# Performance work log

Measured on AMD Instinct MI355X. Metric: run time of the kernel, lower is better.

Reference implementation:

```python
import jax, jax.numpy as jnp
import numpy as np

EPS = 1e-6
LOG2PI = float(np.log(2.0 * np.pi))


def gauss_lp(x, mu, lv):
    """Diagonal Gaussian log prob. x:[B,D], mu:[K,D], lv:[K,D] -> [B,K]."""
    inv_var = jnp.exp(-lv)                          # [K,D]
    d = x[:, None, :] - mu[None, :, :]              # [B,K,D]
    quad = jnp.sum(d * d * inv_var[None], axis=-1)  # [B,K]
    logdet = jnp.sum(lv, axis=-1)[None]             # [1,K]
    D = mu.shape[-1]
    return -0.5 * (quad + logdet + D * LOG2PI)


def setup_inputs() -> dict:
    key = jax.random.key(0)
    ks = jax.random.split(key, 9)
    T, B, S, A, OBS, CTL = 200, 256, 256, 16, 128, 16
    return {
        "x": jax.random.normal(ks[0], (T, B, OBS), jnp.float32),
        "u": jax.random.normal(ks[1], (T, B, CTL), jnp.float32),
        "obs_mu": jax.random.normal(ks[2], (S, OBS), jnp.float32),
        "obs_lv": 0.1 * jax.random.normal(ks[3], (S, OBS), jnp.float32),
        "ctl_mu": jax.random.normal(ks[4], (A, CTL), jnp.float32),
        "ctl_lv": 0.1 * jax.random.normal(ks[5], (A, CTL), jnp.float32),
        "trans_logits": jax.random.normal(ks[6], (A, S, S), jnp.float32),
        "pi0_logits": jax.random.normal(ks[7], (S,), jnp.float32),
        "act_prior": jax.random.normal(ks[8], (S, A), jnp.float32),
    }


def reference(x, u, obs_mu, obs_lv, ctl_mu, ctl_lv, trans_logits, pi0_logits, act_prior):
    """HMM forward algorithm (ContinuousGaussianHMM._forward).

    Returns:
      alpha_b: [T, B, S] state forward messages
      alpha_a: [T-1, B, A] action forward messages
    """
    S = obs_mu.shape[0]
    trans = jax.nn.softmax(trans_logits, axis=-1)      # [A,S,S]
    log_pi0 = jax.nn.log_softmax(pi0_logits)           # [S]

    # t = 0: initial state prior + observation likelihood
    b0 = jax.nn.softmax(gauss_lp(x[0], obs_mu, obs_lv) + log_pi0[None], axis=-1)  # [B,S]

    def step(b, xu):
        x_t, u_t = xu
        # action prior from belief: softmax(b @ act_prior)
        a_prior = jax.nn.softmax(b @ act_prior, axis=-1)                           # [B,A]
        # ctl_model.infer: posterior over actions given control u_t
        a_t = jax.nn.softmax(gauss_lp(u_t, ctl_mu, ctl_lv) + jnp.log(a_prior + EPS), axis=-1)  # [B,A]
        # action-conditioned transition applied to belief
        m = jnp.einsum('bi,kij->bkj', b, trans)                                    # [B,A,S]
        # original: sum_i(trans*b + eps) => einsum + S*eps
        logp_z = jnp.log(jnp.einsum('bk,bkj->bj', a_t, m) + S * EPS)               # [B,S]
        b_next = jax.nn.softmax(gauss_lp(x_t, obs_mu, obs_lv) + logp_z, axis=-1)   # [B,S]
        return b_next, (b_next, a_t)

    _, (bs, a_s) = jax.lax.scan(step, b0, (x[1:], u[:-1]))
    alpha_b = jnp.concatenate([b0[None], bs], axis=0)   # [T,B,S]
    alpha_a = a_s                                       # [T-1,B,A]
    return alpha_b, alpha_a
```

## Files before the change

### kernel.cpp

```cpp
#include <hip/hip_runtime.h>
#include <hip/hip_bf16.h>
#include <stdint.h>

#define T_STEPS 200
#define BATCH   256
#define NS      256
#define NA      16
#define DOBS    128
#define DCTL    16
#define LOG2PI  1.8378770664093453f
#define EPS_F   1e-6f

typedef float f32x4 __attribute__((ext_vector_type(4)));
typedef short s16x8 __attribute__((ext_vector_type(8)));
typedef short s16x4 __attribute__((ext_vector_type(4)));

static __device__ __forceinline__ unsigned short f2bf(float f) {
    union { float f; unsigned u; } v; v.f = f;
    unsigned u = v.u;
    u += 0x7fffu + ((u >> 16) & 1u);
    return (unsigned short)(u >> 16);
}

static __device__ __forceinline__ float ld_agent(const float* p) {
    return __hip_atomic_load(p, __ATOMIC_RELAXED, __HIP_MEMORY_SCOPE_AGENT);
}
static __device__ __forceinline__ void st_agent(float* p, float v) {
    __hip_atomic_store(p, v, __ATOMIC_RELAXED, __HIP_MEMORY_SCOPE_AGENT);
}

__global__ __launch_bounds__(128) void k_prep_obs(const float* __restrict__ obs_mu,
                                                  const float* __restrict__ obs_lv,
                                                  float* __restrict__ WT,
                                                  float* __restrict__ Cs) {
    int s = blockIdx.x, d = threadIdx.x;
    float lv = obs_lv[s * DOBS + d];
    float mu = obs_mu[s * DOBS + d];
    float iv = expf(-lv);
    WT[d * NS + s]          = -0.5f * iv;
    WT[(DOBS + d) * NS + s] = mu * iv;
    float part = mu * mu * iv + lv;
    for (int m = 1; m < 64; m <<= 1) part += __shfl_xor(part, m, 64);
    __shared__ float red[2];
    if ((threadIdx.x & 63) == 0) red[threadIdx.x >> 6] = part;
    __syncthreads();
    if (threadIdx.x == 0) Cs[s] = -0.5f * (red[0] + red[1] + DOBS * LOG2PI);
}

__global__ __launch_bounds__(256) void k_prep_ctl(const float* __restrict__ cmu,
                                                  const float* __restrict__ clv,
                                                  float* __restrict__ cw1,
                                                  float* __restrict__ cw2,
                                                  float* __restrict__ cc) {
    int t = threadIdx.x;
    int a = t >> 4, d = t & 15;
    float lv = clv[a * DCTL + d];
    float mu = cmu[a * DCTL + d];
    float iv = expf(-lv);
    cw1[t] = -0.5f * iv;
    cw2[t] = mu * iv;
    float part = mu * mu * iv + lv;
    for (int m = 1; m < 16; m <<= 1) part += __shfl_xor(part, m, 64);
    if (d == 0) cc[a] = -0.5f * (part + DCTL * LOG2PI);
}

__global__ __launch_bounds__(64) void k_prep_pi0(const float* __restrict__ pl,
                                                 float* __restrict__ lpi0) {
    int l = threadIdx.x;
    float v[4]; float m = -1e30f;
    for (int k = 0; k < 4; k++) { v[k] = pl[l + 64 * k]; m = fmaxf(m, v[k]); }
    for (int mm = 1; mm < 64; mm <<= 1) m = fmaxf(m, __shfl_xor(m, mm, 64));
    float ssum = 0.f;
    for (int k = 0; k < 4; k++) ssum += expf(v[k] - m);
    for (int mm = 1; mm < 64; mm <<= 1) ssum += __shfl_xor(ssum, mm, 64);
    float ls = logf(ssum);
    for (int k = 0; k < 4; k++) lpi0[l + 64 * k] = v[k] - m - ls;
}

__global__ __launch_bounds__(512) void k_zero(int* __restrict__ f) {
    f[threadIdx.x] = 0;
}

__global__ __launch_bounds__(256) void k_trans(const float* __restrict__ tl,
                                               __hip_bfloat16* __restrict__ TRf) {
    int wave = threadIdx.x >> 6, lane = threadIdx.x & 63;
    int row = blockIdx.x * 4 + wave;
    int a = row >> 8, i = row & 255;
    const float* src = tl + (size_t)row * NS;
    float v[4]; float m = -1e30f;
    for (int k = 0; k < 4; k++) { v[k] = src[lane + 64 * k]; m = fmaxf(m, v[k]); }
    for (int mm = 1; mm < 64; mm <<= 1) m = fmaxf(m, __shfl_xor(m, mm, 64));
    float ssum = 0.f; float ev[4];
    for (int k = 0; k < 4; k++) { ev[k] = expf(v[k] - m); ssum += ev[k]; }
    for (int mm = 1; mm < 64; mm <<= 1) ssum += __shfl_xor(ssum, mm, 64);
    float inv = 1.f / ssum;
    int kk = i >> 5;
    int lsub = ((i >> 3) & 3) * 16 + a;
    int e = i & 7;
    for (int k = 0; k < 4; k++) {
        int j = lane + 64 * k;
        float p = ev[k] * inv;
        TRf[((size_t)(j * 8 + kk) * 64 + lsub) * 8 + e] = __float2bfloat16(p);
    }
}

__global__ __launch_bounds__(64) void k_prep_ap(const float* __restrict__ ap,
                                                __hip_bfloat16* __restrict__ APh,
                                                __hip_bfloat16* __restrict__ APl) {
    int kk = blockIdx.x, lane = threadIdx.x;
    for (int e = 0; e < 8; e++) {
        int i = kk * 32 + (lane >> 4) * 8 + e;
        int a = lane & 15;
        float v = ap[i * NA + a];
        __hip_bfloat16 hb = __float2bfloat16(v);
        float hi = __bfloat162float(hb);
        APh[(kk * 64 + lane) * 8 + e] = hb;
        APl[(kk * 64 + lane) * 8 + e] = __float2bfloat16(v - hi);
    }
}

__global__ __launch_bounds__(256) void k_obslp(const float* __restrict__ x,
                                               const float* __restrict__ WT,
                                               const float* __restrict__ Cs,
                                               float* __restrict__ obs) {
    __shared__ float f[32 * 256];
    int r0 = blockIdx.x * 32;
    for (int idx = threadIdx.x; idx < 32 * DOBS; idx += 256) {
        int r = idx >> 7, d = idx & 127;
        float v = x[(size_t)(r0 + r) * DOBS + d];
        f[r * 256 + d] = v * v;
        f[r * 256 + 128 + d] = v;
    }
    __syncthreads();
    int s = threadIdx.x;
    float acc[32];
#pragma unroll
    for (int r = 0; r < 32; r++) acc[r] = 0.f;
    for (int d4 = 0; d4 < 64; d4++) {
        float w0 = WT[(d4 * 4 + 0) * NS + s];
        float w1 = WT[(d4 * 4 + 1) * NS + s];
        float w2 = WT[(d4 * 4 + 2) * NS + s];
        float w3 = WT[(d4 * 4 + 3) * NS + s];
#pragma unroll
        for (int r = 0; r < 32; r++) {
            f32x4 fv = *reinterpret_cast<const f32x4*>(&f[r * 256 + d4 * 4]);
            acc[r] += fv.x * w0 + fv.y * w1 + fv.z * w2 + fv.w * w3;
        }
    }
    float c = Cs[s];
#pragma unroll
    for (int r = 0; r < 32; r++) obs[(size_t)(r0 + r) * NS + s] = acc[r] + c;
}

__global__ __launch_bounds__(256) void k_ctllp(const float* __restrict__ u,
                                               const float* __restrict__ cw1,
                                               const float* __restrict__ cw2,
                                               const float* __restrict__ cc,
                                               float* __restrict__ ctl) {
    int idx = blockIdx.x * 256 + threadIdx.x;
    int r = idx >> 4, a = idx & 15;
    const float* ur = u + (size_t)r * DCTL;
    const float* w1 = cw1 + a * DCTL;
    const float* w2 = cw2 + a * DCTL;
    float acc = cc[a];
#pragma unroll
    for (int d = 0; d < 16; d++) {
        float uv = ur[d];
        acc += uv * uv * w1[d] + uv * w2[d];
    }
    ctl[idx] = acc;
}

struct ScanArgs {
    const float* obs;
    const float* ctlp;
    const float* lpi0;
    const __hip_bfloat16* TRf;
    const __hip_bfloat16* APh;
    const __hip_bfloat16* APl;
    float* lgA;
    float* lgB;
    float* out_ab;
    float* out_aa;
    int*   flags;
};

__global__ __launch_bounds__(256, 1) void k_scan_p(ScanArgs A) {
    const int bid  = blockIdx.x;
    const int bt   = bid >> 4;
    const int jt   = bid & 15;
    const int tid  = threadIdx.x;
    const int wv   = tid >> 6, lane = tid & 63;
    const int kgrp = lane >> 4, arow = lane & 15;
    const int b0   = bt * 16;
    int* flag = A.flags + bt * 32;

    __shared__ short AFL[8][16][32];

    s16x8 bfr[4][8];
#pragma unroll
    for (int q = 0; q < 4; q++) {
        int ct = jt * 16 + wv * 4 + q;
#pragma unroll
        for (int kk = 0; kk < 8; kk++)
            bfr[q][kk] = *((const s16x8*)A.TRf + (size_t)(ct * 8 + kk) * 64 + lane);
    }
    s16x8 aph[8], apl[8];
#pragma unroll
    for (int kk = 0; kk < 8; kk++) {
        aph[kk] = *((const s16x8*)A.APh + kk * 64 + lane);
        apl[kk] = *((const s16x8*)A.APl + kk * 64 + lane);
    }
    f32x4 lp0 = *(const f32x4*)&A.lpi0[lane * 4];

    for (int s = 0; s < T_STEPS - 1; s++) {
        const float* lin = (s & 1) ? A.lgB : A.lgA;
        float*       lout = (s & 1) ? A.lgA : A.lgB;

        float obs_pf[16];
#pragma unroll
        for (int q2 = 0; q2 < 4; q2++)
#pragma unroll
            for (int r = 0; r < 4; r++)
                obs_pf[q2 * 4 + r] =
                    A.obs[((size_t)(s + 1) * BATCH + b0 + kgrp * 4 + r) * NS + jt * 16 + wv * 4 + q2];

        if (s > 0) {
            if (tid == 0) {
                int tgt = 16 * s;
                while (__hip_atomic_load(flag, __ATOMIC_RELAXED, __HIP_MEMORY_SCOPE_AGENT) < tgt)
                    __builtin_amdgcn_s_sleep(2);
            }
            __syncthreads();
        }

        float vr[4][4];
        if (s == 0) {
#pragma unroll
            for (int q = 0; q < 4; q++) {
                int bb = b0 + wv * 4 + q;
                f32x4 o = *(const f32x4*)&A.obs[(size_t)bb * NS + lane * 4];
                vr[q][0] = o.x + lp0.x; vr[q][1] = o.y + lp0.y;
                vr[q][2] = o.z + lp0.z; vr[q][3] = o.w + lp0.w;
            }
        } else {
#pragma unroll
            for (int q = 0; q < 4; q++) {
                const float* rp = &lin[(size_t)(b0 + wv * 4 + q) * NS + lane * 4];
#pragma unroll
                for (int k = 0; k < 4; k++) vr[q][k] = ld_agent(rp + k);
            }
        }
#pragma unroll
        for (int q = 0; q < 4; q++) {
            int r = wv * 4 + q, bb = b0 + r;
            float m = fmaxf(fmaxf(vr[q][0], vr[q][1]), fmaxf(vr[q][2], vr[q][3]));
            for (int mm = 1; mm < 64; mm <<= 1) m = fmaxf(m, __shfl_xor(m, mm, 64));
            float e0 = __expf(vr[q][0] - m), e1 = __expf(vr[q][1] - m);
            float e2 = __expf(vr[q][2] - m), e3 = __expf(vr[q][3] - m);
            float ss = (e0 + e1) + (e2 + e3);
            for (int mm = 1; mm < 64; mm <<= 1) ss += __shfl_xor(ss, mm, 64);
            float inv = 1.f / ss;
            float p0 = e0 * inv, p1 = e1 * inv, p2 = e2 * inv, p3 = e3 * inv;
            if ((lane >> 2) == jt) {
                f32x4 pv = {p0, p1, p2, p3};
                *(f32x4*)&A.out_ab[((size_t)s * BATCH + bb) * NS + lane * 4] = pv;
            }
            s16x4 sv;
            sv[0] = (short)f2bf(p0); sv[1] = (short)f2bf(p1);
            sv[2] = (short)f2bf(p2); sv[3] = (short)f2bf(p3);
            *(s16x4*)&AFL[lane >> 3][r][(lane & 7) * 4] = sv;
        }
        __syncthreads();

        s16x8 afr[8];
#pragma unroll
        for (int kk = 0; kk < 8; kk++)
            afr[kk] = *(const s16x8*)&AFL[kk][arow][kgrp * 8];

        f32x4 g = {0.f, 0.f, 0.f, 0.f};
#pragma unroll
        for (int kk = 0; kk < 8; kk++)
            g = __builtin_amdgcn_mfma_f32_16x16x32_bf16(afr[kk], aph[kk], g, 0, 0, 0);
#pragma unroll
        for (int kk = 0; kk < 8; kk++)
            g = __builtin_amdgcn_mfma_f32_16x16x32_bf16(afr[kk], apl[kk], g, 0, 0, 0);

        float at[4];
#pragma unroll
        for (int q = 0; q < 4; q++) {
            float gv = g[q];
            float m = gv;
            for (int mm = 1; mm < 16; mm <<= 1) m = fmaxf(m, __shfl_xor(m, mm, 64));
            float e1 = __expf(gv - m);
            float s1 = e1;
            for (int mm = 1; mm < 16; mm <<= 1) s1 += __shfl_xor(s1, mm, 64);
            float apr = e1 / s1;
            float al = A.ctlp[((size_t)s * BATCH + b0 + kgrp * 4 + q) * NA + arow]
                       + __logf(apr + EPS_F);
            float m2 = al;
            for (int mm = 1; mm < 16; mm <<= 1) m2 = fmaxf(m2, __shfl_xor(m2, mm, 64));
            float e2 = __expf(al - m2);
            float s2 = e2;
            for (int mm = 1; mm < 16; mm <<= 1) s2 += __shfl_xor(s2, mm, 64);
            at[q] = e2 / s2;
            if (jt == 0)
                A.out_aa[((size_t)s * BATCH + b0 + kgrp * 4 + q) * NA + arow] = at[q];
        }

#pragma unroll
        for (int q2 = 0; q2 < 4; q2++) {
            int ct = jt * 16 + wv * 4 + q2;
            f32x4 acc = {0.f, 0.f, 0.f, 0.f};
#pragma unroll
            for (int kk = 0; kk < 8; kk++)
                acc = __builtin_amdgcn_mfma_f32_16x16x32_bf16(afr[kk], bfr[q2][kk], acc, 0, 0, 0);
#pragma unroll
            for (int r = 0; r < 4; r++) {
                float vv = acc[r] * at[r];
                for (int mm = 1; mm < 16; mm <<= 1) vv += __shfl_xor(vv, mm, 64);
                if (arow == 0) {
                    float lz = __logf(vv + NS * EPS_F);
                    st_agent(&lout[(size_t)(b0 + kgrp * 4 + r) * NS + ct],
                             obs_pf[q2 * 4 + r] + lz);
                }
            }
        }

        asm volatile("s_waitcnt vmcnt(0)" ::: "memory");
        __syncthreads();
        if (tid == 0)
            __hip_atomic_fetch_add(flag, 1, __ATOMIC_RELAXED, __HIP_MEMORY_SCOPE_AGENT);
    }

    if (tid == 0) {
        int tgt = 16 * (T_STEPS - 1);
        while (__hip_atomic_load(flag, __ATOMIC_RELAXED, __HIP_MEMORY_SCOPE_AGENT) < tgt)
            __builtin_amdgcn_s_sleep(2);
    }
    __syncthreads();
    const float* lin = ((T_STEPS - 1) & 1) ? A.lgB : A.lgA;
#pragma unroll
    for (int q = 0; q < 4; q++) {
        int r = wv * 4 + q, bb = b0 + r;
        float v0 = ld_agent(&lin[(size_t)bb * NS + lane * 4 + 0]);
        float v1 = ld_agent(&lin[(size_t)bb * NS + lane * 4 + 1]);
        float v2 = ld_agent(&lin[(size_t)bb * NS + lane * 4 + 2]);
        float v3 = ld_agent(&lin[(size_t)bb * NS + lane * 4 + 3]);
        float m = fmaxf(fmaxf(v0, v1), fmaxf(v2, v3));
        for (int mm = 1; mm < 64; mm <<= 1) m = fmaxf(m, __shfl_xor(m, mm, 64));
        float e0 = __expf(v0 - m), e1 = __expf(v1 - m);
        float e2 = __expf(v2 - m), e3 = __expf(v3 - m);
        float ss = (e0 + e1) + (e2 + e3);
        for (int mm = 1; mm < 64; mm <<= 1) ss += __shfl_xor(ss, mm, 64);
        float inv = 1.f / ss;
        if ((lane >> 2) == jt) {
            f32x4 pv = {e0 * inv, e1 * inv, e2 * inv, e3 * inv};
            *(f32x4*)&A.out_ab[((size_t)(T_STEPS - 1) * BATCH + bb) * NS + lane * 4] = pv;
        }
    }
}

extern "C" void kernel_launch(void* const* d_in, const int* in_sizes, int n_in,
                              void* d_out, int out_size, void* d_ws, size_t ws_size,
                              hipStream_t stream) {
    const float* x            = (const float*)d_in[0];
    const float* u            = (const float*)d_in[1];
    const float* obs_mu       = (const float*)d_in[2];
    const float* obs_lv       = (const float*)d_in[3];
    const float* ctl_mu       = (const float*)d_in[4];
    const float* ctl_lv       = (const float*)d_in[5];
    const float* trans_logits = (const float*)d_in[6];
    const float* pi0_logits   = (const float*)d_in[7];
    const float* act_prior    = (const float*)d_in[8];

    float* out_ab = (float*)d_out;
    float* out_aa = out_ab + (size_t)T_STEPS * BATCH * NS;

    char* w = (char*)d_ws;
    size_t off = 0;
    auto alloc = [&](size_t bytes) -> void* {
        void* pp = w + off;
        off += (bytes + 255) & ~(size_t)255;
        return pp;
    };
    float* WT   = (float*)alloc((size_t)256 * 256 * 4);
    float* Cs   = (float*)alloc(256 * 4);
    float* cw1  = (float*)alloc(256 * 4);
    float* cw2  = (float*)alloc(256 * 4);
    float* cc   = (float*)alloc(16 * 4);
    float* lpi0 = (float*)alloc(256 * 4);
    __hip_bfloat16* TRf = (__hip_bfloat16*)alloc((size_t)4096 * 256 * 2);
    __hip_bfloat16* APh = (__hip_bfloat16*)alloc((size_t)8 * 64 * 8 * 2);
    __hip_bfloat16* APl = (__hip_bfloat16*)alloc((size_t)8 * 64 * 8 * 2);
    float* obs  = (float*)alloc((size_t)T_STEPS * BATCH * NS * 4);
    float* ctlp = (float*)alloc((size_t)(T_STEPS - 1) * BATCH * NA * 4);
    float* lgA  = (float*)alloc((size_t)BATCH * NS * 4);
    float* lgB  = (float*)alloc((size_t)BATCH * NS * 4);
    int*   flags = (int*)alloc(16 * 32 * 4);
    if (off > ws_size) return;

    k_zero<<<1, 512, 0, stream>>>(flags);
    k_prep_obs<<<256, 128, 0, stream>>>(obs_mu, obs_lv, WT, Cs);
    k_prep_ctl<<<1, 256, 0, stream>>>(ctl_mu, ctl_lv, cw1, cw2, cc);
    k_prep_pi0<<<1, 64, 0, stream>>>(pi0_logits, lpi0);
    k_trans<<<1024, 256, 0, stream>>>(trans_logits, TRf);
    k_prep_ap<<<8, 64, 0, stream>>>(act_prior, APh, APl);
    k_obslp<<<1600, 256, 0, stream>>>(x, WT, Cs, obs);
    k_ctllp<<<3184, 256, 0, stream>>>(u, cw1, cw2, cc, ctlp);

    ScanArgs args;
    args.obs = obs; args.ctlp = ctlp; args.lpi0 = lpi0;
    args.TRf = TRf; args.APh = APh; args.APl = APl;
    args.lgA = lgA; args.lgB = lgB;
    args.out_ab = out_ab; args.out_aa = out_aa; args.flags = flags;
    k_scan_p<<<256, 256, 0, stream>>>(args);
}
```

Baseline: 2.320 ms.

## Replace shared atomic counter with per-block step flags and coalesced cache-bypassing exchange

The persistent scan kernel now has each block publish its own step counter instead of doing a fetch_add on one shared counter per batch tile. Waiters poll all 16 flags with vector loads and take the minimum. Per-step logits are staged in LDS and written as a single coalesced dwordx4 store per row, and reads use vectorized sc0 sc1 loads in place of scalar atomic loads. The control log-prob load is prefetched before the wait, and the LDS belief tile is XOR-swizzled to avoid bank conflicts. The aim is to shorten the inter-block synchronization latency on the critical path, at the cost of inline asm memory-coherence assumptions.

```diff
diff --git a/kernel.cpp b/kernel.cpp
--- a/kernel.cpp
+++ b/kernel.cpp
@@ -10,8 +10,10 @@
 #define DCTL    16
 #define LOG2PI  1.8378770664093453f
 #define EPS_F   1e-6f
+#define MINI(a,b) ((a)<(b)?(a):(b))
 
 typedef float f32x4 __attribute__((ext_vector_type(4)));
+typedef int   i32x4 __attribute__((ext_vector_type(4)));
 typedef short s16x8 __attribute__((ext_vector_type(8)));
 typedef short s16x4 __attribute__((ext_vector_type(4)));
 
@@ -22,11 +24,37 @@
     return (unsigned short)(u >> 16);
 }
 
-static __device__ __forceinline__ float ld_agent(const float* p) {
-    return __hip_atomic_load(p, __ATOMIC_RELAXED, __HIP_MEMORY_SCOPE_AGENT);
-}
-static __device__ __forceinline__ void st_agent(float* p, float v) {
-    __hip_atomic_store(p, v, __ATOMIC_RELAXED, __HIP_MEMORY_SCOPE_AGENT);
+static __device__ __forceinline__ void ld4_mall(const float* base,
+                                                f32x4& a, f32x4& b, f32x4& c, f32x4& d) {
+    asm volatile(
+        "global_load_dwordx4 %0, %4, off offset:0 sc0 sc1\n\t"
+        "global_load_dwordx4 %1, %4, off offset:1024 sc0 sc1\n\t"
+        "global_load_dwordx4 %2, %4, off offset:2048 sc0 sc1\n\t"
+        "global_load_dwordx4 %3, %4, off offset:3072 sc0 sc1\n\t"
+        "s_waitcnt vmcnt(0)"
+        : "=&v"(a), "=&v"(b), "=&v"(c), "=&v"(d)
+        : "v"(base)
+        : "memory");
+}
+static __device__ __forceinline__ void st_mall(float* p, f32x4 v) {
+    asm volatile("global_store_dwordx4 %0, %1, off sc0 sc1" :: "v"(p), "v"(v) : "memory");
+}
+static __device__ __forceinline__ int min16(const int* fp) {
+    i32x4 a, b, c, d;
+    asm volatile(
+        "global_load_dwordx4 %0, %4, off offset:0 sc0 sc1\n\t"
+        "global_load_dwordx4 %1, %4, off offset:16 sc0 sc1\n\t"
+        "global_load_dwordx4 %2, %4, off offset:32 sc0 sc1\n\t"
+        "global_load_dwordx4 %3, %4, off offset:48 sc0 sc1\n\t"
+        "s_waitcnt vmcnt(0)"
+        : "=&v"(a), "=&v"(b), "=&v"(c), "=&v"(d)
+        : "v"(fp)
+        : "memory");
+    int m = MINI(MINI(a[0], a[1]), MINI(a[2], a[3]));
+    m = MINI(m, MINI(MINI(b[0], b[1]), MINI(b[2], b[3])));
+    m = MINI(m, MINI(MINI(c[0], c[1]), MINI(c[2], c[3])));
+    m = MINI(m, MINI(MINI(d[0], d[1]), MINI(d[2], d[3])));
+    return m;
 }
 
 __global__ __launch_bounds__(128) void k_prep_obs(const float* __restrict__ obs_mu,
@@ -77,7 +105,7 @@
     for (int k = 0; k < 4; k++) lpi0[l + 64 * k] = v[k] - m - ls;
 }
 
-__global__ __launch_bounds__(512) void k_zero(int* __restrict__ f) {
+__global__ __launch_bounds__(256) void k_zero(int* __restrict__ f) {
     f[threadIdx.x] = 0;
 }
 
@@ -193,9 +221,10 @@
     const int wv   = tid >> 6, lane = tid & 63;
     const int kgrp = lane >> 4, arow = lane & 15;
     const int b0   = bt * 16;
-    int* flag = A.flags + bt * 32;
-
-    __shared__ short AFL[8][16][32];
+    const int* fp  = A.flags + bt * 16;
+
+    __shared__ __align__(16) char PLb[16 * 512];
+    __shared__ float out_t[16][16];
 
     s16x8 bfr[4][8];
 #pragma unroll
@@ -224,40 +253,35 @@
             for (int r = 0; r < 4; r++)
                 obs_pf[q2 * 4 + r] =
                     A.obs[((size_t)(s + 1) * BATCH + b0 + kgrp * 4 + r) * NS + jt * 16 + wv * 4 + q2];
+        float ctl_pf[4];
+#pragma unroll
+        for (int q = 0; q < 4; q++)
+            ctl_pf[q] = A.ctlp[((size_t)s * BATCH + b0 + kgrp * 4 + q) * NA + arow];
 
         if (s > 0) {
             if (tid == 0) {
-                int tgt = 16 * s;
-                while (__hip_atomic_load(flag, __ATOMIC_RELAXED, __HIP_MEMORY_SCOPE_AGENT) < tgt)
-                    __builtin_amdgcn_s_sleep(2);
+                while (min16(fp) < s) __builtin_amdgcn_s_sleep(1);
             }
             __syncthreads();
         }
 
-        float vr[4][4];
+        f32x4 V[4];
         if (s == 0) {
 #pragma unroll
             for (int q = 0; q < 4; q++) {
-                int bb = b0 + wv * 4 + q;
-                f32x4 o = *(const f32x4*)&A.obs[(size_t)bb * NS + lane * 4];
-                vr[q][0] = o.x + lp0.x; vr[q][1] = o.y + lp0.y;
-                vr[q][2] = o.z + lp0.z; vr[q][3] = o.w + lp0.w;
+                f32x4 o = *(const f32x4*)&A.obs[(size_t)(b0 + wv * 4 + q) * NS + lane * 4];
+                V[q] = o + lp0;
             }
         } else {
-#pragma unroll
-            for (int q = 0; q < 4; q++) {
-                const float* rp = &lin[(size_t)(b0 + wv * 4 + q) * NS + lane * 4];
-#pragma unroll
-                for (int k = 0; k < 4; k++) vr[q][k] = ld_agent(rp + k);
-            }
+            ld4_mall(lin + (size_t)(b0 + wv * 4) * NS + lane * 4, V[0], V[1], V[2], V[3]);
         }
 #pragma unroll
         for (int q = 0; q < 4; q++) {
             int r = wv * 4 + q, bb = b0 + r;
-            float m = fmaxf(fmaxf(vr[q][0], vr[q][1]), fmaxf(vr[q][2], vr[q][3]));
+            float m = fmaxf(fmaxf(V[q].x, V[q].y), fmaxf(V[q].z, V[q].w));
             for (int mm = 1; mm < 64; mm <<= 1) m = fmaxf(m, __shfl_xor(m, mm, 64));
-            float e0 = __expf(vr[q][0] - m), e1 = __expf(vr[q][1] - m);
-            float e2 = __expf(vr[q][2] - m), e3 = __expf(vr[q][3] - m);
+            float e0 = __expf(V[q].x - m), e1 = __expf(V[q].y - m);
+            float e2 = __expf(V[q].z - m), e3 = __expf(V[q].w - m);
             float ss = (e0 + e1) + (e2 + e3);
             for (int mm = 1; mm < 64; mm <<= 1) ss += __shfl_xor(ss, mm, 64);
             float inv = 1.f / ss;
@@ -269,14 +293,17 @@
             s16x4 sv;
             sv[0] = (short)f2bf(p0); sv[1] = (short)f2bf(p1);
             sv[2] = (short)f2bf(p2); sv[3] = (short)f2bf(p3);
-            *(s16x4*)&AFL[lane >> 3][r][(lane & 7) * 4] = sv;
+            *(s16x4*)(PLb + r * 512 + ((lane * 8) ^ ((r & 7) << 4))) = sv;
         }
         __syncthreads();
 
         s16x8 afr[8];
-#pragma unroll
-        for (int kk = 0; kk < 8; kk++)
-            afr[kk] = *(const s16x8*)&AFL[kk][arow][kgrp * 8];
+        {
+            int sw = (arow & 7) << 4;
+#pragma unroll
+            for (int kk = 0; kk < 8; kk++)
+                afr[kk] = *(const s16x8*)(PLb + arow * 512 + ((kk * 64 + kgrp * 16) ^ sw));
+        }
 
         f32x4 g = {0.f, 0.f, 0.f, 0.f};
 #pragma unroll
@@ -296,8 +323,7 @@
             float s1 = e1;
             for (int mm = 1; mm < 16; mm <<= 1) s1 += __shfl_xor(s1, mm, 64);
             float apr = e1 / s1;
-            float al = A.ctlp[((size_t)s * BATCH + b0 + kgrp * 4 + q) * NA + arow]
-                       + __logf(apr + EPS_F);
+            float al = ctl_pf[q] + __logf(apr + EPS_F);
             float m2 = al;
             for (int mm = 1; mm < 16; mm <<= 1) m2 = fmaxf(m2, __shfl_xor(m2, mm, 64));
             float e2 = __expf(al - m2);
@@ -310,7 +336,6 @@
 
 #pragma unroll
         for (int q2 = 0; q2 < 4; q2++) {
-            int ct = jt * 16 + wv * 4 + q2;
             f32x4 acc = {0.f, 0.f, 0.f, 0.f};
 #pragma unroll
             for (int kk = 0; kk < 8; kk++)
@@ -319,38 +344,38 @@
             for (int r = 0; r < 4; r++) {
                 float vv = acc[r] * at[r];
                 for (int mm = 1; mm < 16; mm <<= 1) vv += __shfl_xor(vv, mm, 64);
-                if (arow == 0) {
-                    float lz = __logf(vv + NS * EPS_F);
-                    st_agent(&lout[(size_t)(b0 + kgrp * 4 + r) * NS + ct],
-                             obs_pf[q2 * 4 + r] + lz);
-                }
+                if (arow == 0)
+                    out_t[kgrp * 4 + r][wv * 4 + q2] =
+                        obs_pf[q2 * 4 + r] + __logf(vv + NS * EPS_F);
             }
         }
-
-        asm volatile("s_waitcnt vmcnt(0)" ::: "memory");
         __syncthreads();
-        if (tid == 0)
-            __hip_atomic_fetch_add(flag, 1, __ATOMIC_RELAXED, __HIP_MEMORY_SCOPE_AGENT);
+
+        if (wv == 0) {
+            int row = lane >> 2, cloc = (lane & 3) * 4;
+            f32x4 val = *(const f32x4*)&out_t[row][cloc];
+            st_mall(&lout[(size_t)(b0 + row) * NS + jt * 16 + cloc], val);
+            asm volatile("s_waitcnt vmcnt(0)" ::: "memory");
+            if (lane == 0)
+                __hip_atomic_store(&A.flags[bt * 16 + jt], s + 1,
+                                   __ATOMIC_RELAXED, __HIP_MEMORY_SCOPE_AGENT);
+        }
     }
 
     if (tid == 0) {
-        int tgt = 16 * (T_STEPS - 1);
-        while (__hip_atomic_load(flag, __ATOMIC_RELAXED, __HIP_MEMORY_SCOPE_AGENT) < tgt)
-            __builtin_amdgcn_s_sleep(2);
+        while (min16(fp) < T_STEPS - 1) __builtin_amdgcn_s_sleep(1);
     }
     __syncthreads();
     const float* lin = ((T_STEPS - 1) & 1) ? A.lgB : A.lgA;
+    f32x4 V[4];
+    ld4_mall(lin + (size_t)(b0 + wv * 4) * NS + lane * 4, V[0], V[1], V[2], V[3]);
 #pragma unroll
     for (int q = 0; q < 4; q++) {
-        int r = wv * 4 + q, bb = b0 + r;
-        float v0 = ld_agent(&lin[(size_t)bb * NS + lane * 4 + 0]);
-        float v1 = ld_agent(&lin[(size_t)bb * NS + lane * 4 + 1]);
-        float v2 = ld_agent(&lin[(size_t)bb * NS + lane * 4 + 2]);
-        float v3 = ld_agent(&lin[(size_t)bb * NS + lane * 4 + 3]);
-        float m = fmaxf(fmaxf(v0, v1), fmaxf(v2, v3));
+        int bb = b0 + wv * 4 + q;
+        float m = fmaxf(fmaxf(V[q].x, V[q].y), fmaxf(V[q].z, V[q].w));
         for (int mm = 1; mm < 64; mm <<= 1) m = fmaxf(m, __shfl_xor(m, mm, 64));
-        float e0 = __expf(v0 - m), e1 = __expf(v1 - m);
-        float e2 = __expf(v2 - m), e3 = __expf(v3 - m);
+        float e0 = __expf(V[q].x - m), e1 = __expf(V[q].y - m);
+        float e2 = __expf(V[q].z - m), e3 = __expf(V[q].w - m);
         float ss = (e0 + e1) + (e2 + e3);
         for (int mm = 1; mm < 64; mm <<= 1) ss += __shfl_xor(ss, mm, 64);
         float inv = 1.f / ss;
@@ -397,10 +422,10 @@
     float* ctlp = (float*)alloc((size_t)(T_STEPS - 1) * BATCH * NA * 4);
     float* lgA  = (float*)alloc((size_t)BATCH * NS * 4);
     float* lgB  = (float*)alloc((size_t)BATCH * NS * 4);
-    int*   flags = (int*)alloc(16 * 32 * 4);
+    int*   flags = (int*)alloc(256 * 4);
     if (off > ws_size) return;
 
-    k_zero<<<1, 512, 0, stream>>>(flags);
+    k_zero<<<1, 256, 0, stream>>>(flags);
     k_prep_obs<<<256, 128, 0, stream>>>(obs_mu, obs_lv, WT, Cs);
     k_prep_ctl<<<1, 256, 0, stream>>>(ctl_mu, ctl_lv, cw1, cw2, cc);
     k_prep_pi0<<<1, 64, 0, stream>>>(pi0_logits, lpi0);
```

New measurement: 2.382 ms. 1.03x slower.
